# Kernel tuning notes

Measured on AMD Instinct MI355X. Metric: run time of the kernel, lower is better.

Reference implementation:

```python
import jax, jax.numpy as jnp
import numpy as np

THETA = 2.0  # slope_lim_theta from __init__


def _slope_minmod(f, theta):
    """Minmod-limited slope along last axis; equivalent to the fixed-weight
    Conv1d(1,3,3) with weights [[-t,t,0],[-.5,0,.5],[0,-t,t]] followed by
    minmod over the 3 output channels. Output length = N - 2."""
    df = jnp.diff(f, axis=-1)              # [..., N-1]
    ch0 = theta * df[..., :-1]             # t*(f[i+1]-f[i])
    ch1 = 0.5 * (f[..., 2:] - f[..., :-2]) # 0.5*(f[i+2]-f[i])
    ch2 = theta * df[..., 1:]              # t*(f[i+2]-f[i+1])
    fmin = jnp.minimum(jnp.minimum(ch0, ch1), ch2)
    fmax = jnp.maximum(jnp.maximum(ch0, ch1), ch2)
    # minmod: min|.| if all same sign, else 0 (matches torch clamp/where form)
    return jnp.where(fmin < 0.0, jnp.minimum(fmax, 0.0), fmin)


def setup_inputs() -> dict:
    key = jax.random.key(0)
    k1, k2 = jax.random.split(key)
    B, M, N = 32, 256, 2048
    rho = jax.random.normal(k1, (B, M, N), dtype=jnp.float32)
    v = jax.random.normal(k2, (B, M, N - 4), dtype=jnp.float32)
    return {"rho": rho, "v": v, "axis": 2}


def reference(rho, v, axis):
    rho = jnp.swapaxes(rho, axis, -1)
    v = jnp.swapaxes(v, axis, -1)
    half_slope = 0.5 * _slope_minmod(rho, THETA)     # [..., N-2]
    rho_diff = jnp.diff(rho[..., 1:-1], axis=-1)     # [..., N-3]
    hs_diff = jnp.diff(half_slope, axis=-1)          # [..., N-3]
    result_minus = (rho_diff - hs_diff)[..., 1:]     # [..., N-4]
    result_plus = (rho_diff + hs_diff)[..., :-1]     # [..., N-4]
    delta_rho = jnp.where(v < 0.0, result_minus, result_plus)
    return jnp.swapaxes(v * delta_rho, axis, -1)
```

## Files before the change

### kernel.cpp

```cpp
#include <hip/hip_runtime.h>

#define THETA 2.0f
#define NRHO 2048
#define NOUT 2044

typedef float floatx4 __attribute__((ext_vector_type(4)));

__global__ __launch_bounds__(512) void vprime_stencil_kernel(
    const float* __restrict__ rho,
    const float* __restrict__ v,
    float* __restrict__ out)
{
    const int row = blockIdx.x;
    const int t   = threadIdx.x;

    const float* rrow = rho + (size_t)row * NRHO;

    floatx4 lo = reinterpret_cast<const floatx4*>(rrow)[t];

    if (t < 511) {
        floatx4 hi = reinterpret_cast<const floatx4*>(rrow)[t + 1];

        float x[8] = {lo.x, lo.y, lo.z, lo.w, hi.x, hi.y, hi.z, hi.w};

        float hs[6];
        #pragma unroll
        for (int i = 0; i < 6; ++i) {
            float a  = THETA * (x[i + 1] - x[i]);
            float b  = 0.5f  * (x[i + 2] - x[i]);
            float c  = THETA * (x[i + 2] - x[i + 1]);
            float mn = fminf(fminf(a, b), c);
            float mx = fmaxf(fmaxf(a, b), c);
            float mm = (mn < 0.0f) ? fminf(mx, 0.0f) : mn;
            hs[i] = 0.5f * mm;
        }

        const float* vrow = v   + (size_t)row * NOUT;
        float*       orow = out + (size_t)row * NOUT;

        floatx4 vv = reinterpret_cast<const floatx4*>(vrow)[t];
        float vf[4] = {vv.x, vv.y, vv.z, vv.w};

        floatx4 res;
        #pragma unroll
        for (int j = 0; j < 4; ++j) {
            float rp = (x[j + 2] - x[j + 1]) + (hs[j + 1] - hs[j]);
            float rm = (x[j + 3] - x[j + 2]) - (hs[j + 2] - hs[j + 1]);
            float dr = (vf[j] < 0.0f) ? rm : rp;
            res[j] = vf[j] * dr;
        }

        __builtin_nontemporal_store(res, reinterpret_cast<floatx4*>(orow) + t);
    }
}

extern "C" void kernel_launch(void* const* d_in, const int* in_sizes, int n_in,
                              void* d_out, int out_size, void* d_ws, size_t ws_size,
                              hipStream_t stream) {
    const float* rho = (const float*)d_in[0];
    const float* v   = (const float*)d_in[1];
    float* out       = (float*)d_out;

    const int rows = in_sizes[0] / NRHO;

    vprime_stencil_kernel<<<rows, 512, 0, stream>>>(rho, v, out);
}
```

Baseline: 34.16 us.

## Process four rows per block with eight outputs per thread

Each thread now produces eight outputs instead of four, and each block covers four rows. All loads for the four rows are issued up front to raise memory-level parallelism. This cuts the redundant halo load per output, since each thread reads three float4 of rho for eight outputs instead of two for four. The nontemporal store is replaced with a regular store, and the larger register footprint may reduce occupancy.

```diff
diff --git a/kernel.cpp b/kernel.cpp
--- a/kernel.cpp
+++ b/kernel.cpp
@@ -3,54 +3,68 @@
 #define THETA 2.0f
 #define NRHO 2048
 #define NOUT 2044
+#define RPB  4
 
 typedef float floatx4 __attribute__((ext_vector_type(4)));
 
-__global__ __launch_bounds__(512) void vprime_stencil_kernel(
+__global__ __launch_bounds__(256) void vprime_stencil_kernel(
     const float* __restrict__ rho,
     const float* __restrict__ v,
     float* __restrict__ out)
 {
-    const int row = blockIdx.x;
-    const int t   = threadIdx.x;
+    const int t    = threadIdx.x;
+    const int row0 = blockIdx.x * RPB;
+    const bool full = (t < 255);
 
-    const float* rrow = rho + (size_t)row * NRHO;
+    floatx4 R0[RPB], R1[RPB], R2[RPB], V0[RPB], V1[RPB];
 
-    floatx4 lo = reinterpret_cast<const floatx4*>(rrow)[t];
+    #pragma unroll
+    for (int rr = 0; rr < RPB; ++rr) {
+        const size_t row = row0 + rr;
+        const floatx4* r4 = reinterpret_cast<const floatx4*>(rho + row * NRHO);
+        const floatx4* v4 = reinterpret_cast<const floatx4*>(v   + row * NOUT);
+        R0[rr] = r4[2 * t];
+        R1[rr] = r4[2 * t + 1];
+        R2[rr] = full ? r4[2 * t + 2] : floatx4{0.f, 0.f, 0.f, 0.f};
+        V0[rr] = v4[2 * t];
+        V1[rr] = full ? v4[2 * t + 1] : floatx4{0.f, 0.f, 0.f, 0.f};
+    }
 
-    if (t < 511) {
-        floatx4 hi = reinterpret_cast<const floatx4*>(rrow)[t + 1];
+    #pragma unroll
+    for (int rr = 0; rr < RPB; ++rr) {
+        const size_t row = row0 + rr;
+        floatx4* o4 = reinterpret_cast<floatx4*>(out + row * NOUT);
 
-        float x[8] = {lo.x, lo.y, lo.z, lo.w, hi.x, hi.y, hi.z, hi.w};
+        float x[12] = {R0[rr].x, R0[rr].y, R0[rr].z, R0[rr].w,
+                       R1[rr].x, R1[rr].y, R1[rr].z, R1[rr].w,
+                       R2[rr].x, R2[rr].y, R2[rr].z, R2[rr].w};
 
-        float hs[6];
+        float hs[10];
         #pragma unroll
-        for (int i = 0; i < 6; ++i) {
+        for (int i = 0; i < 10; ++i) {
             float a  = THETA * (x[i + 1] - x[i]);
             float b  = 0.5f  * (x[i + 2] - x[i]);
             float c  = THETA * (x[i + 2] - x[i + 1]);
             float mn = fminf(fminf(a, b), c);
             float mx = fmaxf(fmaxf(a, b), c);
-            float mm = (mn < 0.0f) ? fminf(mx, 0.0f) : mn;
-            hs[i] = 0.5f * mm;
+            hs[i] = 0.5f * ((mn < 0.0f) ? fminf(mx, 0.0f) : mn);
         }
 
-        const float* vrow = v   + (size_t)row * NOUT;
-        float*       orow = out + (size_t)row * NOUT;
+        float vf[8] = {V0[rr].x, V0[rr].y, V0[rr].z, V0[rr].w,
+                       V1[rr].x, V1[rr].y, V1[rr].z, V1[rr].w};
 
-        floatx4 vv = reinterpret_cast<const floatx4*>(vrow)[t];
-        float vf[4] = {vv.x, vv.y, vv.z, vv.w};
-
-        floatx4 res;
+        floatx4 res0, res1;
         #pragma unroll
-        for (int j = 0; j < 4; ++j) {
-            float rp = (x[j + 2] - x[j + 1]) + (hs[j + 1] - hs[j]);
-            float rm = (x[j + 3] - x[j + 2]) - (hs[j + 2] - hs[j + 1]);
-            float dr = (vf[j] < 0.0f) ? rm : rp;
-            res[j] = vf[j] * dr;
+        for (int m = 0; m < 8; ++m) {
+            float rp = (x[m + 2] - x[m + 1]) + (hs[m + 1] - hs[m]);
+            float rm = (x[m + 3] - x[m + 2]) - (hs[m + 2] - hs[m + 1]);
+            float dr = (vf[m] < 0.0f) ? rm : rp;
+            float r  = vf[m] * dr;
+            if (m < 4) res0[m] = r; else res1[m - 4] = r;
         }
 
-        __builtin_nontemporal_store(res, reinterpret_cast<floatx4*>(orow) + t);
+        o4[2 * t] = res0;
+        if (full) o4[2 * t + 1] = res1;
     }
 }
 
@@ -63,5 +77,5 @@
 
     const int rows = in_sizes[0] / NRHO;
 
-    vprime_stencil_kernel<<<rows, 512, 0, stream>>>(rho, v, out);
+    vprime_stencil_kernel<<<rows / RPB, 256, 0, stream>>>(rho, v, out);
 }
```

After: 34.98 us. 1.02x slower.
